# Performance work log

Measured on AMD Instinct MI355X. Metric: run time of the kernel, lower is better.

The kernel has to match this reference:

```python
import jax, jax.numpy as jnp
import numpy as np

N = 100_000      # nodes
E = 1_600_000    # directed edges (before self-loops)
F_IN = 128       # input node features
H = 4            # attention heads
C = 64           # hidden channels (concat=False -> heads averaged)
NEG_SLOPE = 0.2
BN_EPS = 1e-5


def setup_inputs() -> dict:
    key = jax.random.key(0)
    ks = jax.random.split(key, 16)
    s = 0.05
    return {
        "x": jax.random.normal(ks[0], (N, F_IN), dtype=jnp.float32),
        "edge_index": jax.random.randint(ks[1], (2, E), 0, N, dtype=jnp.int64),
        # GAT layer params: layer 0 has F_IN inputs, layers 1..2 have C inputs
        "W0": jax.random.normal(ks[2], (F_IN, H * C), dtype=jnp.float32) * s,
        "Wl": jax.random.normal(ks[3], (2, C, H * C), dtype=jnp.float32) * s,
        "att_src": jax.random.normal(ks[4], (3, H, C), dtype=jnp.float32) * s,
        "att_dst": jax.random.normal(ks[5], (3, H, C), dtype=jnp.float32) * s,
        "conv_bias": jnp.zeros((3, C), dtype=jnp.float32),
        # BatchNorm1d (inference: running stats)
        "bn_gamma": jnp.ones((3, C), dtype=jnp.float32),
        "bn_beta": jnp.zeros((3, C), dtype=jnp.float32),
        "bn_mean": jax.random.normal(ks[6], (3, C), dtype=jnp.float32) * 0.1,
        "bn_var": jax.random.uniform(ks[7], (3, C), dtype=jnp.float32, minval=0.5, maxval=1.5),
        # MLP head
        "lin1_w": jax.random.normal(ks[8], (C, C // 2), dtype=jnp.float32) * s,
        "lin1_b": jnp.zeros((C // 2,), dtype=jnp.float32),
        "lin2_w": jax.random.normal(ks[9], (C // 2, 1), dtype=jnp.float32) * s,
        "lin2_b": jnp.zeros((1,), dtype=jnp.float32),
    }


def _gat_layer(x, src, dst, W, a_src, a_dst, bias):
    # x: [N, Fin] -> h: [N, H, C]
    h = (x @ W).reshape(-1, H, C)
    # per-node attention logits, gathered per edge: [Etot, H]
    e_src = jnp.einsum("nhc,hc->nh", h, a_src)
    e_dst = jnp.einsum("nhc,hc->nh", h, a_dst)
    e = jax.nn.leaky_relu(e_src[src] + e_dst[dst], NEG_SLOPE)
    # softmax over incoming edges of each target node (self-loops guarantee non-empty)
    e_max = jax.ops.segment_max(e, dst, num_segments=N)
    w = jnp.exp(e - e_max[dst])                              # [Etot, H]
    denom = jax.ops.segment_sum(w, dst, num_segments=N)      # [N, H]
    # weighted scatter-add of gathered source features
    msg = h[src] * w[:, :, None]                             # [Etot, H, C]
    out = jax.ops.segment_sum(msg, dst, num_segments=N)      # [N, H, C]
    out = out / denom[:, :, None]
    return out.mean(axis=1) + bias                           # concat=False -> head mean


def reference(x, edge_index, W0, Wl, att_src, att_dst, conv_bias,
              bn_gamma, bn_beta, bn_mean, bn_var,
              lin1_w, lin1_b, lin2_w, lin2_b):
    # add self-loops (PyG GATConv default)
    loop = jnp.arange(N, dtype=edge_index.dtype)
    src = jnp.concatenate([edge_index[0], loop])
    dst = jnp.concatenate([edge_index[1], loop])

    Ws = [W0, Wl[0], Wl[1]]
    for l in range(3):
        x = _gat_layer(x, src, dst, Ws[l], att_src[l], att_dst[l], conv_bias[l])
        x = (x - bn_mean[l]) * (bn_gamma[l] / jnp.sqrt(bn_var[l] + BN_EPS)) + bn_beta[l]
        x = jax.nn.relu(x)  # dropout is identity in inference

    x = jax.nn.relu(x @ lin1_w + lin1_b)
    x = x @ lin2_w + lin2_b
    return x.squeeze(-1)
```

## Files before the change

### kernel.cpp

```cpp
#include <hip/hip_runtime.h>
#include <hip/hip_bf16.h>
#include <cstdint>

#define N_NODES 100000
#define N_EDGES 1600000
#define N_TOT   1700000
#define HEADS   4
#define CH      64
#define HC      256
#define NEG     0.2f
#define BNEPS   1e-5f
#define NPART   8
#define PART_N  12500
#define CHUNK_E 16384

typedef __attribute__((ext_vector_type(8))) short short8;
typedef __attribute__((ext_vector_type(4))) float f32x4;

static __device__ __forceinline__ float lrelu(float x) {
    return x > 0.f ? x : NEG * x;
}
static __device__ __forceinline__ unsigned short f2bf(float f) {
    unsigned int u = __float_as_uint(f);
    unsigned int r = (u + 0x7fffu + ((u >> 16) & 1u)) >> 16;
    return (unsigned short)r;
}
static __device__ __forceinline__ float bflo(unsigned int v) { return __uint_as_float(v << 16); }
static __device__ __forceinline__ float bfhi(unsigned int v) { return __uint_as_float(v & 0xffff0000u); }

__global__ void convert_hist_k(const void* ei,
                               int* __restrict__ src32, int* __restrict__ dst32,
                               int* __restrict__ counts) {
    const int* e32 = (const int*)ei;
    int l = threadIdx.x & 63;
    unsigned long long b = __ballot(e32[2 * l + 1] == 0);
    int is64 = (__popcll(b) >= 48) ? 1 : 0;

    int e = blockIdx.x * 256 + threadIdx.x;
    if (e >= N_TOT) return;
    int s, d;
    if (e < N_EDGES) {
        if (is64) {
            s = (int)((const long long*)ei)[e];
            d = (int)((const long long*)ei)[(long long)N_EDGES + e];
        } else {
            s = ((const int*)ei)[e];
            d = ((const int*)ei)[N_EDGES + e];
        }
    } else { int v = e - N_EDGES; s = v; d = v; }
    src32[e] = s; dst32[e] = d;
    atomicAdd(&counts[d], 1);
}

__global__ void scan_block(const int* in, int* out, int* bsum) {
    __shared__ int sm[256];
    int t = threadIdx.x;
    int i = blockIdx.x * 256 + t;
    int v = (i < N_NODES) ? in[i] : 0;
    int acc = v;
    sm[t] = v; __syncthreads();
    for (int d = 1; d < 256; d <<= 1) {
        int add = (t >= d) ? sm[t - d] : 0;
        __syncthreads();
        acc += add; sm[t] = acc;
        __syncthreads();
    }
    if (i < N_NODES) out[i] = acc - v;
    if (t == 255) bsum[blockIdx.x] = acc;
}

__global__ void scan_bsum(int* bsum, int nb) {
    __shared__ int sm[512];
    int t = threadIdx.x;
    int v = (t < nb) ? bsum[t] : 0;
    int acc = v;
    sm[t] = v; __syncthreads();
    for (int d = 1; d < 512; d <<= 1) {
        int add = (t >= d) ? sm[t - d] : 0;
        __syncthreads();
        acc += add; sm[t] = acc;
        __syncthreads();
    }
    if (t < nb) bsum[t] = acc - v;
}

__global__ void scan_add(int* off, const int* bsum, int* fill) {
    int i = blockIdx.x * 256 + threadIdx.x;
    if (i < N_NODES) {
        int v = off[i] + bsum[blockIdx.x];
        off[i] = v; fill[i] = v;
    }
    if (i == 0) off[N_NODES] = N_TOT;
}

__global__ void scatter_part_k(const int* __restrict__ src32, const int* __restrict__ dst32,
                               int* __restrict__ fill, int* __restrict__ csr) {
    int part = blockIdx.x & (NPART - 1), chunk = blockIdx.x / NPART;
    int lo = part * PART_N, hi = lo + PART_N;
    int base = chunk * CHUNK_E;
    int end = min(base + CHUNK_E, N_TOT);
    for (int i = base + threadIdx.x; i < end; i += 256) {
        int d = dst32[i];
        if (d >= lo && d < hi) {
            int s = src32[i];
            int pos = atomicAdd(&fill[d], 1);
            csr[pos] = s;
        }
    }
}

template<int K, bool ABF16>
__global__ __launch_bounds__(256) void gemm_mfma_k(const void* __restrict__ Ain,
                                                   const float* __restrict__ Wf,
                                                   const float* __restrict__ as,
                                                   const float* __restrict__ ad,
                                                   unsigned short* __restrict__ hb,
                                                   float* __restrict__ es,
                                                   float* __restrict__ ed, int ntiles) {
    __shared__ __align__(16) unsigned short Bs[256 * K];
    __shared__ __align__(16) unsigned short As[64 * K];
    int t = threadIdx.x;

    for (int idx4 = t; idx4 < K * 64; idx4 += 256) {
        int k = idx4 >> 6;
        int c = (idx4 & 63) * 4;
        float4 wv = *(const float4*)(Wf + (size_t)k * HC + c);
        Bs[((c + 0) * K + k) ^ (((c + 0) & 7) << 3)] = f2bf(wv.x);
        Bs[((c + 1) * K + k) ^ (((c + 1) & 7) << 3)] = f2bf(wv.y);
        Bs[((c + 2) * K + k) ^ (((c + 2) & 7) << 3)] = f2bf(wv.z);
        Bs[((c + 3) * K + k) ^ (((c + 3) & 7) << 3)] = f2bf(wv.w);
    }

    int w = t >> 6, lane = t & 63;
    int c16 = lane & 15, kg = lane >> 4;
    int swz = (c16 & 7) << 3;
    float asv[4], adv[4];
    #pragma unroll
    for (int ct = 0; ct < 4; ++ct) {
        asv[ct] = as[w * 64 + ct * 16 + c16];
        adv[ct] = ad[w * 64 + ct * 16 + c16];
    }
    __syncthreads();

    for (int tile = blockIdx.x; tile < ntiles; tile += gridDim.x) {
        int bm = tile * 64;
        #pragma unroll
        for (int i = 0; i < (64 * K / 8) / 256; ++i) {
            int cidx = i * 256 + t;
            int row = cidx / (K / 8);
            int ks = (cidx % (K / 8)) * 8;
            int grow = bm + row;
            uint4 pk = make_uint4(0, 0, 0, 0);
            if (grow < N_NODES) {
                if (ABF16) {
                    pk = *(const uint4*)((const unsigned short*)Ain + (size_t)grow * K + ks);
                } else {
                    const float* Af = (const float*)Ain + (size_t)grow * K + ks;
                    float4 v0 = *(const float4*)Af;
                    float4 v1 = *(const float4*)(Af + 4);
                    pk.x = (unsigned)f2bf(v0.x) | ((unsigned)f2bf(v0.y) << 16);
                    pk.y = (unsigned)f2bf(v0.z) | ((unsigned)f2bf(v0.w) << 16);
                    pk.z = (unsigned)f2bf(v1.x) | ((unsigned)f2bf(v1.y) << 16);
                    pk.w = (unsigned)f2bf(v1.z) | ((unsigned)f2bf(v1.w) << 16);
                }
            }
            *(uint4*)(&As[(row * K + ks) ^ ((row & 7) << 3)]) = pk;
        }
        __syncthreads();

        f32x4 acc[4][4];
        #pragma unroll
        for (int i = 0; i < 4; ++i)
            #pragma unroll
            for (int j = 0; j < 4; ++j) acc[i][j] = (f32x4)(0.f);

        #pragma unroll
        for (int kc = 0; kc < K / 32; ++kc) {
            int ko = kc * 32 + kg * 8;
            short8 af[4], bf[4];
            #pragma unroll
            for (int rs = 0; rs < 4; ++rs)
                af[rs] = *(const short8*)(&As[((16 * rs + c16) * K + ko) ^ swz]);
            #pragma unroll
            for (int ct = 0; ct < 4; ++ct) {
                int col = w * 64 + ct * 16 + c16;
                bf[ct] = *(const short8*)(&Bs[(col * K + ko) ^ swz]);
            }
            #pragma unroll
            for (int rs = 0; rs < 4; ++rs)
                #pragma unroll
                for (int ct = 0; ct < 4; ++ct)
                    acc[rs][ct] = __builtin_amdgcn_mfma_f32_16x16x32_bf16(af[rs], bf[ct], acc[rs][ct], 0, 0, 0);
        }

        #pragma unroll
        for (int rs = 0; rs < 4; ++rs) {
            float esr[4], edr[4];
            #pragma unroll
            for (int reg = 0; reg < 4; ++reg) {
                float s = 0.f, d = 0.f;
                #pragma unroll
                for (int ct = 0; ct < 4; ++ct) {
                    s += acc[rs][ct][reg] * asv[ct];
                    d += acc[rs][ct][reg] * adv[ct];
                }
                #pragma unroll
                for (int sh = 1; sh < 16; sh <<= 1) {
                    s += __shfl_xor(s, sh);
                    d += __shfl_xor(d, sh);
                }
                esr[reg] = s; edr[reg] = d;
            }
            if (c16 == 0) {
                int r0 = bm + rs * 16 + kg * 4;
                #pragma unroll
                for (int reg = 0; reg < 4; ++reg) {
                    if (r0 + reg < N_NODES) {
                        es[(size_t)(r0 + reg) * 4 + w] = esr[reg];
                        ed[(size_t)(r0 + reg) * 4 + w] = edr[reg];
                    }
                }
            }
        }
        __syncthreads();

        #pragma unroll
        for (int rs = 0; rs < 4; ++rs) {
            #pragma unroll
            for (int ct = 0; ct < 4; ++ct)
                #pragma unroll
                for (int reg = 0; reg < 4; ++reg)
                    As[(kg * 4 + reg) * 256 + w * 64 + ct * 16 + c16] = f2bf(acc[rs][ct][reg]);
            __syncthreads();
            int row16 = t >> 4, cseg = (t & 15) * 16;
            int grow = bm + rs * 16 + row16;
            if (grow < N_NODES) {
                uint4 v0 = *(const uint4*)(&As[row16 * 256 + cseg]);
                uint4 v1 = *(const uint4*)(&As[row16 * 256 + cseg + 8]);
                *(uint4*)(hb + (size_t)grow * HC + cseg) = v0;
                *(uint4*)(hb + (size_t)grow * HC + cseg + 8) = v1;
            }
            __syncthreads();
        }
    }
}

template<bool OUTBF16>
__global__ __launch_bounds__(256) void aggregate_k(const unsigned short* __restrict__ h,
                                                   const float* __restrict__ es,
                                                   const float* __restrict__ ed,
                                                   const int* __restrict__ off,
                                                   const int* __restrict__ csr,
                                                   const float* __restrict__ bias,
                                                   const float* __restrict__ g,
                                                   const float* __restrict__ bb,
                                                   const float* __restrict__ mu,
                                                   const float* __restrict__ var,
                                                   void* __restrict__ xout) {
    __shared__ float wbuf[4][64][4];
    __shared__ int   sbuf[4][64];
    int wv = threadIdx.x >> 6;
    int lane = threadIdx.x & 63;
    int wid = blockIdx.x * 4 + wv;
    if (wid >= N_NODES) return;

    int s0 = off[wid], s1 = off[wid + 1];
    float4 edv = *(const float4*)(ed + (size_t)wid * 4);

    int half = lane >> 5;
    int sub  = lane & 31;
    int head = sub >> 3;
    float ds0 = 0.f, ds1 = 0.f, ds2 = 0.f, ds3 = 0.f;
    float a0 = 0.f, a1 = 0.f, a2 = 0.f, a3 = 0.f, a4 = 0.f, a5 = 0.f, a6 = 0.f, a7 = 0.f;
    const unsigned short* hsub = h + sub * 8;

    for (int base = s0; base < s1; base += 64) {
        int e = base + lane;
        float w0 = 0.f, w1 = 0.f, w2 = 0.f, w3 = 0.f;
        int s = 0;
        if (e < s1) {
            s = csr[e];
            float4 ev = *(const float4*)(es + (size_t)s * 4);
            w0 = __expf(fminf(lrelu(ev.x + edv.x), 80.f));
            w1 = __expf(fminf(lrelu(ev.y + edv.y), 80.f));
            w2 = __expf(fminf(lrelu(ev.z + edv.z), 80.f));
            w3 = __expf(fminf(lrelu(ev.w + edv.w), 80.f));
        }
        ds0 += w0; ds1 += w1; ds2 += w2; ds3 += w3;
        *(float4*)(&wbuf[wv][lane][0]) = make_float4(w0, w1, w2, w3);
        sbuf[wv][lane] = s;
        asm volatile("" ::: "memory");

        int cnt = min(64, s1 - base);
        int jj = half;
        int scur = (jj < cnt) ? sbuf[wv][jj] : sbuf[wv][0];
        float wcur = (jj < cnt) ? wbuf[wv][jj][head] : 0.f;
        uint4 hv = *(const uint4*)(hsub + (size_t)scur * HC);
        for (int j = 0; j < cnt; j += 2) {
            int jn = j + 2 + half;
            int snx = (jn < cnt) ? sbuf[wv][jn] : sbuf[wv][0];
            float wnx = (jn < cnt) ? wbuf[wv][jn][head] : 0.f;
            uint4 hn = *(const uint4*)(hsub + (size_t)snx * HC);
            a0 = fmaf(wcur, bflo(hv.x), a0); a1 = fmaf(wcur, bfhi(hv.x), a1);
            a2 = fmaf(wcur, bflo(hv.y), a2); a3 = fmaf(wcur, bfhi(hv.y), a3);
            a4 = fmaf(wcur, bflo(hv.z), a4); a5 = fmaf(wcur, bfhi(hv.z), a5);
            a6 = fmaf(wcur, bflo(hv.w), a6); a7 = fmaf(wcur, bfhi(hv.w), a7);
            hv = hn; wcur = wnx;
        }
        asm volatile("" ::: "memory");
    }

    a0 += __shfl_xor(a0, 32); a1 += __shfl_xor(a1, 32);
    a2 += __shfl_xor(a2, 32); a3 += __shfl_xor(a3, 32);
    a4 += __shfl_xor(a4, 32); a5 += __shfl_xor(a5, 32);
    a6 += __shfl_xor(a6, 32); a7 += __shfl_xor(a7, 32);

    #pragma unroll
    for (int d = 1; d < 64; d <<= 1) {
        ds0 += __shfl_xor(ds0, d); ds1 += __shfl_xor(ds1, d);
        ds2 += __shfl_xor(ds2, d); ds3 += __shfl_xor(ds3, d);
    }
    float den = head == 0 ? ds0 : head == 1 ? ds1 : head == 2 ? ds2 : ds3;
    float inv = 1.f / den;
    a0 *= inv; a1 *= inv; a2 *= inv; a3 *= inv;
    a4 *= inv; a5 *= inv; a6 *= inv; a7 *= inv;

    a0 += __shfl_xor(a0, 8);  a1 += __shfl_xor(a1, 8);
    a2 += __shfl_xor(a2, 8);  a3 += __shfl_xor(a3, 8);
    a4 += __shfl_xor(a4, 8);  a5 += __shfl_xor(a5, 8);
    a6 += __shfl_xor(a6, 8);  a7 += __shfl_xor(a7, 8);
    a0 += __shfl_xor(a0, 16); a1 += __shfl_xor(a1, 16);
    a2 += __shfl_xor(a2, 16); a3 += __shfl_xor(a3, 16);
    a4 += __shfl_xor(a4, 16); a5 += __shfl_xor(a5, 16);
    a6 += __shfl_xor(a6, 16); a7 += __shfl_xor(a7, 16);

    if (lane < 8) {
        int c = lane * 8;
        float av[8] = {a0, a1, a2, a3, a4, a5, a6, a7};
        float4 bi0 = *(const float4*)(bias + c), bi1 = *(const float4*)(bias + c + 4);
        float4 gv0 = *(const float4*)(g + c),    gv1 = *(const float4*)(g + c + 4);
        float4 bv0 = *(const float4*)(bb + c),   bv1 = *(const float4*)(bb + c + 4);
        float4 mv0 = *(const float4*)(mu + c),   mv1 = *(const float4*)(mu + c + 4);
        float4 vv0 = *(const float4*)(var + c),  vv1 = *(const float4*)(var + c + 4);
        float bia[8] = {bi0.x, bi0.y, bi0.z, bi0.w, bi1.x, bi1.y, bi1.z, bi1.w};
        float gg[8]  = {gv0.x, gv0.y, gv0.z, gv0.w, gv1.x, gv1.y, gv1.z, gv1.w};
        float be[8]  = {bv0.x, bv0.y, bv0.z, bv0.w, bv1.x, bv1.y, bv1.z, bv1.w};
        float mm[8]  = {mv0.x, mv0.y, mv0.z, mv0.w, mv1.x, mv1.y, mv1.z, mv1.w};
        float vv[8]  = {vv0.x, vv0.y, vv0.z, vv0.w, vv1.x, vv1.y, vv1.z, vv1.w};
        float o[8];
        #pragma unroll
        for (int k = 0; k < 8; ++k) {
            float t0 = (av[k] * 0.25f + bia[k] - mm[k]) * (gg[k] * rsqrtf(vv[k] + BNEPS)) + be[k];
            o[k] = fmaxf(t0, 0.f);
        }
        if (OUTBF16) {
            uint4 pk;
            pk.x = (unsigned)f2bf(o[0]) | ((unsigned)f2bf(o[1]) << 16);
            pk.y = (unsigned)f2bf(o[2]) | ((unsigned)f2bf(o[3]) << 16);
            pk.z = (unsigned)f2bf(o[4]) | ((unsigned)f2bf(o[5]) << 16);
            pk.w = (unsigned)f2bf(o[6]) | ((unsigned)f2bf(o[7]) << 16);
            *(uint4*)((unsigned short*)xout + (size_t)wid * CH + c) = pk;
        } else {
            *(float4*)((float*)xout + (size_t)wid * CH + c)     = make_float4(o[0], o[1], o[2], o[3]);
            *(float4*)((float*)xout + (size_t)wid * CH + c + 4) = make_float4(o[4], o[5], o[6], o[7]);
        }
    }
}

__global__ __launch_bounds__(256) void mlp_k(const float* __restrict__ x,
                                             const float* __restrict__ w1,
                                             const float* __restrict__ b1,
                                             const float* __restrict__ w2,
                                             const float* __restrict__ b2,
                                             float* __restrict__ out) {
    __shared__ float w1s[CH * 32];
    __shared__ float w2s[32];
    __shared__ float b1s[32];
    int t = threadIdx.x;
    for (int i = t; i < CH * 32; i += 256) w1s[i] = w1[i];
    if (t < 32) { w2s[t] = w2[t]; b1s[t] = b1[t]; }
    __syncthreads();
    int n = blockIdx.x * 256 + t;
    if (n >= N_NODES) return;
    float y[32];
    #pragma unroll
    for (int j = 0; j < 32; ++j) y[j] = b1s[j];
    const float* xr = x + (size_t)n * CH;
    for (int c4 = 0; c4 < 16; ++c4) {
        float4 xv = *(const float4*)(xr + c4 * 4);
        const float* wr = &w1s[c4 * 4 * 32];
        #pragma unroll
        for (int j = 0; j < 32; ++j)
            y[j] += xv.x * wr[j] + xv.y * wr[32 + j] + xv.z * wr[64 + j] + xv.w * wr[96 + j];
    }
    float o = b2[0];
    #pragma unroll
    for (int j = 0; j < 32; ++j) o += fmaxf(y[j], 0.f) * w2s[j];
    out[n] = o;
}

extern "C" void kernel_launch(void* const* d_in, const int* in_sizes, int n_in,
                              void* d_out, int out_size, void* d_ws, size_t ws_size,
                              hipStream_t stream) {
    const float* x0    = (const float*)d_in[0];
    const void*  ei    = d_in[1];
    const float* W0    = (const float*)d_in[2];
    const float* Wl    = (const float*)d_in[3];
    const float* asrc  = (const float*)d_in[4];
    const float* adst  = (const float*)d_in[5];
    const float* cbias = (const float*)d_in[6];
    const float* bng   = (const float*)d_in[7];
    const float* bnb   = (const float*)d_in[8];
    const float* bnm   = (const float*)d_in[9];
    const float* bnv   = (const float*)d_in[10];
    const float* l1w   = (const float*)d_in[11];
    const float* l1b   = (const float*)d_in[12];
    const float* l2w   = (const float*)d_in[13];
    const float* l2b   = (const float*)d_in[14];
    float* out = (float*)d_out;

    char* p = (char*)d_ws;
    auto alloc = [&](size_t bytes) { char* r = p; p += (bytes + 255) & ~(size_t)255; return r; };
    unsigned short* hb   = (unsigned short*)alloc((size_t)N_NODES * HC * 2);
    unsigned short* xb0  = (unsigned short*)alloc((size_t)N_NODES * CH * 2);
    unsigned short* xb1  = (unsigned short*)alloc((size_t)N_NODES * CH * 2);
    float* xf32 = (float*)alloc((size_t)N_NODES * CH * 4);
    float* es   = (float*)alloc((size_t)N_NODES * 4 * 4);
    float* ed   = (float*)alloc((size_t)N_NODES * 4 * 4);
    int* counts = (int*)alloc((size_t)N_NODES * 4);
    int* off    = (int*)alloc((size_t)(N_NODES + 1) * 4);
    int* fill   = (int*)alloc((size_t)N_NODES * 4);
    int* bsum   = (int*)alloc(512 * 4);
    int* src32  = (int*)alloc((size_t)N_TOT * 4);
    int* dst32  = (int*)alloc((size_t)N_TOT * 4);
    int* csr    = (int*)alloc((size_t)N_TOT * 4);

    int nbScan = (N_NODES + 255) / 256;
    int nchunk = (N_TOT + CHUNK_E - 1) / CHUNK_E;
    int ntiles = (N_NODES + 63) / 64;
    hipMemsetAsync(counts, 0, (size_t)N_NODES * 4, stream);
    convert_hist_k<<<(N_TOT + 255) / 256, 256, 0, stream>>>(ei, src32, dst32, counts);
    scan_block<<<nbScan, 256, 0, stream>>>(counts, off, bsum);
    scan_bsum<<<1, 512, 0, stream>>>(bsum, nbScan);
    scan_add<<<nbScan, 256, 0, stream>>>(off, bsum, fill);
    scatter_part_k<<<nchunk * NPART, 256, 0, stream>>>(src32, dst32, fill, csr);

    int nagg = (N_NODES + 3) / 4;
    gemm_mfma_k<128, false><<<512, 256, 0, stream>>>(x0, W0, asrc, adst, hb, es, ed, ntiles);
    aggregate_k<true><<<nagg, 256, 0, stream>>>(hb, es, ed, off, csr,
        cbias, bng, bnb, bnm, bnv, xb0);
    gemm_mfma_k<64, true><<<1024, 256, 0, stream>>>(xb0, Wl, asrc + HC, adst + HC, hb, es, ed, ntiles);
    aggregate_k<true><<<nagg, 256, 0, stream>>>(hb, es, ed, off, csr,
        cbias + CH, bng + CH, bnb + CH, bnm + CH, bnv + CH, xb1);
    gemm_mfma_k<64, true><<<1024, 256, 0, stream>>>(xb1, Wl + (size_t)CH * HC, asrc + 2 * HC, adst + 2 * HC, hb, es, ed, ntiles);
    aggregate_k<false><<<nagg, 256, 0, stream>>>(hb, es, ed, off, csr,
        cbias + 2 * CH, bng + 2 * CH, bnb + 2 * CH, bnm + 2 * CH, bnv + 2 * CH, xf32);

    mlp_k<<<(N_NODES + 255) / 256, 256, 0, stream>>>(xf32, l1w, l1b, l2w, l2b, out);
}
```

Before: 698.5 us.

## Deepen gather prefetch and use packed FMA in GAT aggregation; retune GEMM grids

The aggregation inner loop now keeps two feature rows in flight instead of one. It pads the shared edge buffers with zeroed sentinel slots so the loop no longer needs per-iteration bounds checks. The per-edge accumulation uses v_pk_fma_f32 inline asm on paired floats, roughly halving FMA instruction count. The GEMM launches also use larger grids (782/1563 blocks) to cover more tiles concurrently. The changes trade extra registers and asm-constrained scheduling for more latency hiding on the random row gathers.

```diff
diff --git a/kernel.cpp b/kernel.cpp
--- a/kernel.cpp
+++ b/kernel.cpp
@@ -16,6 +16,7 @@
 
 typedef __attribute__((ext_vector_type(8))) short short8;
 typedef __attribute__((ext_vector_type(4))) float f32x4;
+typedef __attribute__((ext_vector_type(2))) float f32x2;
 
 static __device__ __forceinline__ float lrelu(float x) {
     return x > 0.f ? x : NEG * x;
@@ -257,13 +258,18 @@
                                                    const float* __restrict__ mu,
                                                    const float* __restrict__ var,
                                                    void* __restrict__ xout) {
-    __shared__ float wbuf[4][64][4];
-    __shared__ int   sbuf[4][64];
+    __shared__ float wbuf[4][68][4];
+    __shared__ int   sbuf[4][68];
     int wv = threadIdx.x >> 6;
     int lane = threadIdx.x & 63;
     int wid = blockIdx.x * 4 + wv;
     if (wid >= N_NODES) return;
 
+    if (lane < 4) {
+        sbuf[wv][64 + lane] = 0;
+        *(float4*)(&wbuf[wv][64 + lane][0]) = make_float4(0.f, 0.f, 0.f, 0.f);
+    }
+
     int s0 = off[wid], s1 = off[wid + 1];
     float4 edv = *(const float4*)(ed + (size_t)wid * 4);
 
@@ -271,7 +277,9 @@
     int sub  = lane & 31;
     int head = sub >> 3;
     float ds0 = 0.f, ds1 = 0.f, ds2 = 0.f, ds3 = 0.f;
-    float a0 = 0.f, a1 = 0.f, a2 = 0.f, a3 = 0.f, a4 = 0.f, a5 = 0.f, a6 = 0.f, a7 = 0.f;
+    f32x2 acc2[8];
+    #pragma unroll
+    for (int i = 0; i < 8; ++i) acc2[i] = (f32x2)(0.f);
     const unsigned short* hsub = h + sub * 8;
 
     for (int base = s0; base < s1; base += 64) {
@@ -291,24 +299,35 @@
         sbuf[wv][lane] = s;
         asm volatile("" ::: "memory");
 
-        int cnt = min(64, s1 - base);
-        int jj = half;
-        int scur = (jj < cnt) ? sbuf[wv][jj] : sbuf[wv][0];
-        float wcur = (jj < cnt) ? wbuf[wv][jj][head] : 0.f;
-        uint4 hv = *(const uint4*)(hsub + (size_t)scur * HC);
-        for (int j = 0; j < cnt; j += 2) {
-            int jn = j + 2 + half;
-            int snx = (jn < cnt) ? sbuf[wv][jn] : sbuf[wv][0];
-            float wnx = (jn < cnt) ? wbuf[wv][jn][head] : 0.f;
-            uint4 hn = *(const uint4*)(hsub + (size_t)snx * HC);
-            a0 = fmaf(wcur, bflo(hv.x), a0); a1 = fmaf(wcur, bfhi(hv.x), a1);
-            a2 = fmaf(wcur, bflo(hv.y), a2); a3 = fmaf(wcur, bfhi(hv.y), a3);
-            a4 = fmaf(wcur, bflo(hv.z), a4); a5 = fmaf(wcur, bfhi(hv.z), a5);
-            a6 = fmaf(wcur, bflo(hv.w), a6); a7 = fmaf(wcur, bfhi(hv.w), a7);
-            hv = hn; wcur = wnx;
+        int cnt2 = (min(64, s1 - base) + 1) & ~1;
+        int sA = sbuf[wv][half];
+        float wA = wbuf[wv][half][head];
+        int sB = sbuf[wv][2 + half];
+        float wB = wbuf[wv][2 + half][head];
+        uint4 hA = *(const uint4*)(hsub + (size_t)sA * HC);
+        uint4 hB = *(const uint4*)(hsub + (size_t)sB * HC);
+        for (int j = 0; j < cnt2; j += 2) {
+            int jn = j + 4 + half;
+            int sC = sbuf[wv][jn];
+            float wC = wbuf[wv][jn][head];
+            uint4 hC = *(const uint4*)(hsub + (size_t)sC * HC);
+            f32x2 wp = { wA, wA };
+            f32x2 p0 = { bflo(hA.x), bfhi(hA.x) };
+            f32x2 p1 = { bflo(hA.y), bfhi(hA.y) };
+            f32x2 p2 = { bflo(hA.z), bfhi(hA.z) };
+            f32x2 p3 = { bflo(hA.w), bfhi(hA.w) };
+            asm("v_pk_fma_f32 %0, %1, %2, %0" : "+v"(acc2[0]) : "v"(p0), "v"(wp));
+            asm("v_pk_fma_f32 %0, %1, %2, %0" : "+v"(acc2[1]) : "v"(p1), "v"(wp));
+            asm("v_pk_fma_f32 %0, %1, %2, %0" : "+v"(acc2[2]) : "v"(p2), "v"(wp));
+            asm("v_pk_fma_f32 %0, %1, %2, %0" : "+v"(acc2[3]) : "v"(p3), "v"(wp));
+            hA = hB; wA = wB;
+            hB = hC; wB = wC;
         }
         asm volatile("" ::: "memory");
     }
+
+    float a0 = acc2[0][0], a1 = acc2[0][1], a2 = acc2[1][0], a3 = acc2[1][1];
+    float a4 = acc2[2][0], a5 = acc2[2][1], a6 = acc2[3][0], a7 = acc2[3][1];
 
     a0 += __shfl_xor(a0, 32); a1 += __shfl_xor(a1, 32);
     a2 += __shfl_xor(a2, 32); a3 += __shfl_xor(a3, 32);
@@ -446,13 +465,13 @@
     scatter_part_k<<<nchunk * NPART, 256, 0, stream>>>(src32, dst32, fill, csr);
 
     int nagg = (N_NODES + 3) / 4;
-    gemm_mfma_k<128, false><<<512, 256, 0, stream>>>(x0, W0, asrc, adst, hb, es, ed, ntiles);
+    gemm_mfma_k<128, false><<<782, 256, 0, stream>>>(x0, W0, asrc, adst, hb, es, ed, ntiles);
     aggregate_k<true><<<nagg, 256, 0, stream>>>(hb, es, ed, off, csr,
         cbias, bng, bnb, bnm, bnv, xb0);
-    gemm_mfma_k<64, true><<<1024, 256, 0, stream>>>(xb0, Wl, asrc + HC, adst + HC, hb, es, ed, ntiles);
+    gemm_mfma_k<64, true><<<1563, 256, 0, stream>>>(xb0, Wl, asrc + HC, adst + HC, hb, es, ed, ntiles);
     aggregate_k<true><<<nagg, 256, 0, stream>>>(hb, es, ed, off, csr,
         cbias + CH, bng + CH, bnb + CH, bnm + CH, bnv + CH, xb1);
-    gemm_mfma_k<64, true><<<1024, 256, 0, stream>>>(xb1, Wl + (size_t)CH * HC, asrc + 2 * HC, adst + 2 * HC, hb, es, ed, ntiles);
+    gemm_mfma_k<64, true><<<1563, 256, 0, stream>>>(xb1, Wl + (size_t)CH * HC, asrc + 2 * HC, adst + 2 * HC, hb, es, ed, ntiles);
     aggregate_k<false><<<nagg, 256, 0, stream>>>(hb, es, ed, off, csr,
         cbias + 2 * CH, bng + 2 * CH, bnb + 2 * CH, bnm + 2 * CH, bnv + 2 * CH, xf32);
 
```

Result: slower. 736.1 us (+5.4%).
